# Kernel optimization log

Hardware: AMD Instinct MI355X
Metric: run time of the kernel (lower is better)

The kernel has to match this reference:

```python
import jax, jax.numpy as jnp
import numpy as np

NHEADS = 16


def setup_inputs() -> dict:
    key = jax.random.key(0)
    ks = jax.random.split(key, 5)
    B, S, D = 2, 2048, 1024
    x = jax.random.normal(ks[0], (B, S, D), dtype=jnp.float32)
    W_packed = jax.random.normal(ks[1], (3 * D, D), dtype=jnp.float32) * (1.0 / np.sqrt(D))
    b_packed = jax.random.normal(ks[2], (3 * D,), dtype=jnp.float32) * 0.02
    W_out = jax.random.normal(ks[3], (D, D), dtype=jnp.float32) * (1.0 / np.sqrt(D))
    b_out = jax.random.normal(ks[4], (D,), dtype=jnp.float32) * 0.02
    return {"x": x, "W_packed": W_packed, "b_packed": b_packed, "W_out": W_out, "b_out": b_out}


def reference(x, W_packed, b_packed, W_out, b_out):
    B, S, D = x.shape
    H = NHEADS
    hd = D // H
    # packed QKV projection (self-attention: q is k is v)
    qkv = x @ W_packed.T + b_packed                       # [B,S,3D]
    q, k, v = jnp.split(qkv, 3, axis=-1)

    def heads(t):
        return t.reshape(B, S, H, hd).transpose(0, 2, 1, 3)  # [B,H,S,hd]

    q, k, v = map(heads, (q, k, v))

    # ALiBi slopes per flex path: exp2(-(h+1)*8/H)
    slopes = jnp.exp2(-(jnp.arange(1, H + 1, dtype=x.dtype) * (8.0 / H)))  # [H]
    pos = jnp.arange(S)
    rel = (pos[None, :] - pos[:, None]).astype(x.dtype)    # kv_idx - q_idx, [S,S]
    bias = slopes[:, None, None] * rel                     # [H,S,S]
    causal = pos[None, :] <= pos[:, None]                  # allowed positions
    neg = jnp.finfo(x.dtype).min
    attn_mask = jnp.where(causal[None, :, :], bias, neg)   # [H,S,S]

    scale = 1.0 / np.sqrt(hd)
    scores = jnp.einsum("bhqd,bhkd->bhqk", q, k) * scale + attn_mask[None]
    attn = jax.nn.softmax(scores, axis=-1)
    out = jnp.einsum("bhqk,bhkd->bhqd", attn, v)           # [B,H,S,hd]
    out = out.transpose(0, 2, 1, 3).reshape(B, S, D)
    return out @ W_out.T + b_out
```

## Files before the change

kernel.cpp:

```cpp
#include <hip/hip_runtime.h>

typedef float f32x4 __attribute__((ext_vector_type(4)));
typedef __bf16 bf16x8 __attribute__((ext_vector_type(8)));
typedef unsigned short u16;

__device__ __forceinline__ f32x4 mfma16(bf16x8 a, bf16x8 b, f32x4 c) {
  return __builtin_amdgcn_mfma_f32_16x16x32_bf16(a, b, c, 0, 0, 0);
}

__device__ __forceinline__ void gll16(const void* g, void* l) {
  __builtin_amdgcn_global_load_lds(
      (const __attribute__((address_space(1))) void*)g,
      (__attribute__((address_space(3))) void*)l, 16, 0, 0);
}

__global__ void cvt_kernel(const float* __restrict__ in, __bf16* __restrict__ out, int n8) {
  int idx = blockIdx.x * blockDim.x + threadIdx.x;
  int stride = gridDim.x * blockDim.x;
  for (int i = idx; i < n8; i += stride) {
    const float* p = in + (size_t)i * 8;
    f32x4 a = *(const f32x4*)p;
    f32x4 b = *(const f32x4*)(p + 4);
    bf16x8 r;
#pragma unroll
    for (int j = 0; j < 4; ++j) {
      r[j] = (__bf16)a[j];
      r[4 + j] = (__bf16)b[j];
    }
    *(bf16x8*)(out + (size_t)i * 8) = r;
  }
}

template <int BM, int BN, int MODE>
__global__ __launch_bounds__(256, 4) void gemm_bt(
    const u16* __restrict__ A, const u16* __restrict__ B,
    const float* __restrict__ bias, float* __restrict__ Cout,
    __bf16* __restrict__ qb, __bf16* __restrict__ kp, __bf16* __restrict__ vp,
    int M, int N, int K, int mtiles) {
  constexpr int MREP = BM / 32;
  constexpr int NREP = BN / 32;
  constexpr int LA = BM / 64;
  constexpr int LB = BN / 64;
  __shared__ u16 lA[2 * BM * 32];
  __shared__ u16 lB[2 * BN * 32];
  const int tid = threadIdx.x;
  const int wid = tid >> 6;
  const int lane = tid & 63;
  const int lr = lane & 15;
  const int lg = lane >> 4;

  const int nwg = gridDim.x;
  const int lid = blockIdx.x;
  const int sw = (lid & 7) * (nwg >> 3) + (lid >> 3);
  const int bm = (sw % mtiles) * BM;
  const int bn = (sw / mtiles) * BN;

  const int wm = (wid >> 1) * (BM / 2);
  const int wn = (wid & 1) * (BN / 2);

  f32x4 acc[MREP][NREP] = {};

  auto stage = [&](int bf, int kt) {
    char* baseA = (char*)lA + bf * (BM * 64);
    char* baseB = (char*)lB + bf * (BN * 64);
#pragma unroll
    for (int j = 0; j < LA; ++j) {
      int off = (tid + j * 256) * 16;
      gll16(A + (size_t)(bm + (off >> 6)) * K + kt + ((off & 63) >> 1),
            baseA + off);
    }
#pragma unroll
    for (int j = 0; j < LB; ++j) {
      int off = (tid + j * 256) * 16;
      gll16(B + (size_t)(bn + (off >> 6)) * K + kt + ((off & 63) >> 1),
            baseB + off);
    }
  };

  int buf = 0;
  stage(0, 0);
  for (int kt = 0; kt < K; kt += 32) {
    __syncthreads();
    if (kt + 32 < K) stage(buf ^ 1, kt + 32);
    const u16* cA = lA + buf * BM * 32;
    const u16* cB = lB + buf * BN * 32;
    bf16x8 af[MREP], bfr[NREP];
#pragma unroll
    for (int mt = 0; mt < MREP; ++mt)
      af[mt] = *(const bf16x8*)&cA[(wm + mt * 16 + lr) * 32 + lg * 8];
#pragma unroll
    for (int nt = 0; nt < NREP; ++nt)
      bfr[nt] = *(const bf16x8*)&cB[(wn + nt * 16 + lr) * 32 + lg * 8];
#pragma unroll
    for (int mt = 0; mt < MREP; ++mt)
#pragma unroll
      for (int nt = 0; nt < NREP; ++nt)
        acc[mt][nt] = mfma16(af[mt], bfr[nt], acc[mt][nt]);
    buf ^= 1;
  }

#pragma unroll
  for (int nt = 0; nt < NREP; ++nt) {
    int col = bn + wn + nt * 16 + lr;
    float bv = bias[col];
#pragma unroll
    for (int mt = 0; mt < MREP; ++mt) {
#pragma unroll
      for (int r = 0; r < 4; ++r) {
        int row = bm + wm + mt * 16 + lg * 4 + r;
        float val = acc[mt][nt][r] + bv;
        if (MODE == 0) {
          Cout[(size_t)row * N + col] = val;
        } else {
          __bf16 bx = (__bf16)val;
          int b = row >> 11, s = row & 2047;
          int third = col >> 10, hd = col & 1023;
          int h = hd >> 6, d = hd & 63;
          if (third == 0) {
            qb[(size_t)row * 1024 + hd] = bx;
          } else {
            int bh = b * 16 + h, t = s >> 6, sr = s & 63;
            size_t tb = ((size_t)(bh * 32 + t)) * 4096;
            if (third == 1)
              kp[tb + (sr >> 4) * 1024 + (d >> 5) * 512 + ((d >> 3) & 3) * 128 +
                 (sr & 15) * 8 + (d & 7)] = bx;
            else
              vp[tb + (d >> 4) * 1024 + (sr >> 5) * 512 + ((sr >> 3) & 3) * 128 +
                 (d & 15) * 8 + (sr & 7)] = bx;
          }
        }
      }
    }
  }
}

__global__ __launch_bounds__(64, 4) void attn_kernel(
    const __bf16* __restrict__ qb, const __bf16* __restrict__ kp,
    const __bf16* __restrict__ vp, __bf16* __restrict__ aout) {
  __shared__ __bf16 p_lds[16][72];
  const int lane = threadIdx.x & 63;
  const int lr = lane & 15;
  const int lg = lane >> 4;

  const int lid = blockIdx.x;
  const int xcd = lid & 7;
  const int rest = lid >> 3;
  const int bh = xcd * 4 + (rest & 3);
  const int a16 = 127 - (rest >> 2);
  const int b = bh >> 4, h = bh & 15;
  const int qr0 = a16 * 16;
  const int ntl = (a16 >> 2) + 1;

  const float LOG2E = 1.4426950408889634f;
  const float c1 = 0.125f * LOG2E;
  const float c2 = exp2f(-(float)(h + 1) * 0.5f) * LOG2E;

  bf16x8 ones;
#pragma unroll
  for (int j = 0; j < 8; ++j) ones[j] = (__bf16)1.0f;

  const u16* ktiles = (const u16*)kp + (size_t)bh * 32 * 4096;
  const u16* vtiles = (const u16*)vp + (size_t)bh * 32 * 4096;

  const __bf16* qrow = qb + (size_t)(b * 2048 + qr0 + lr) * 1024 + h * 64;
  bf16x8 qf0 = *(const bf16x8*)(qrow + lg * 8);
  bf16x8 qf1 = *(const bf16x8*)(qrow + 32 + lg * 8);

  float m[4], l[4], cq[4];
  f32x4 o[4];
#pragma unroll
  for (int r = 0; r < 4; ++r) {
    m[r] = 0.f;
    l[r] = 0.f;
    cq[r] = c2 * (float)(qr0 + lg * 4 + r);
  }
#pragma unroll
  for (int dt = 0; dt < 4; ++dt) o[dt] = (f32x4){0.f, 0.f, 0.f, 0.f};

  for (int t = 0; t < ntl; ++t) {
    const u16* kb = ktiles + (size_t)t * 4096;
    const u16* vb = vtiles + (size_t)t * 4096;
    const int kv = t * 64;
    const bool last = (t == ntl - 1);

    bf16x8 ka[8], va[8];
#pragma unroll
    for (int j = 0; j < 8; ++j)
      ka[j] = *(const bf16x8*)(kb + j * 512 + lane * 8);
#pragma unroll
    for (int j = 0; j < 8; ++j)
      va[j] = *(const bf16x8*)(vb + j * 512 + lane * 8);

    f32x4 s[4];
#pragma unroll
    for (int nt = 0; nt < 4; ++nt) {
      f32x4 tt = (f32x4){0.f, 0.f, 0.f, 0.f};
      tt = mfma16(qf0, ka[nt * 2], tt);
      tt = mfma16(qf1, ka[nt * 2 + 1], tt);
      s[nt] = tt;
    }

#pragma unroll
    for (int nt = 0; nt < 4; ++nt) {
      float bnt = c2 * (float)(kv + nt * 16 + lr);
#pragma unroll
      for (int r = 0; r < 4; ++r)
        s[nt][r] = __builtin_fmaf(s[nt][r], c1, bnt - cq[r]);
    }
    if (last) {
#pragma unroll
      for (int nt = 0; nt < 4; ++nt) {
        float kf = (float)(kv + nt * 16 + lr);
#pragma unroll
        for (int r = 0; r < 4; ++r) {
          float qi = (float)(qr0 + lg * 4 + r);
          if (kf > qi) s[nt][r] = -1e30f;
        }
      }
    }

    float pm[4];
#pragma unroll
    for (int r = 0; r < 4; ++r)
      pm[r] = fmaxf(fmaxf(s[0][r], s[1][r]), fmaxf(s[2][r], s[3][r]));
    bool ok = (pm[0] <= m[0] + 8.f) && (pm[1] <= m[1] + 8.f) &&
              (pm[2] <= m[2] + 8.f) && (pm[3] <= m[3] + 8.f);
    if (!__all(ok)) {
#pragma unroll
      for (int r = 0; r < 4; ++r)
#pragma unroll
        for (int d = 1; d < 16; d <<= 1)
          pm[r] = fmaxf(pm[r], __shfl_xor(pm[r], d));
#pragma unroll
      for (int r = 0; r < 4; ++r) {
        float mn = fmaxf(m[r], pm[r]);
        float fac = __builtin_amdgcn_exp2f(m[r] - mn);
        m[r] = mn;
        l[r] *= fac;
#pragma unroll
        for (int dt = 0; dt < 4; ++dt) o[dt][r] *= fac;
      }
    }

#pragma unroll
    for (int nt = 0; nt < 4; ++nt)
#pragma unroll
      for (int r = 0; r < 4; ++r) {
        float e = __builtin_amdgcn_exp2f(s[nt][r] - m[r]);
        p_lds[lg * 4 + r][nt * 16 + lr] = (__bf16)e;
      }

    bf16x8 pa0 = *(const bf16x8*)&p_lds[lr][lg * 8];
    bf16x8 pa1 = *(const bf16x8*)&p_lds[lr][32 + lg * 8];

    {
      f32x4 tt = (f32x4){0.f, 0.f, 0.f, 0.f};
      tt = mfma16(pa0, ones, tt);
      tt = mfma16(pa1, ones, tt);
#pragma unroll
      for (int r = 0; r < 4; ++r) l[r] += tt[r];
    }

#pragma unroll
    for (int dt = 0; dt < 4; ++dt) {
      o[dt] = mfma16(pa0, va[dt * 2], o[dt]);
      o[dt] = mfma16(pa1, va[dt * 2 + 1], o[dt]);
    }
  }

#pragma unroll
  for (int dt = 0; dt < 4; ++dt)
#pragma unroll
    for (int r = 0; r < 4; ++r) {
      float val = o[dt][r] / l[r];
      aout[(size_t)(b * 2048 + qr0 + lg * 4 + r) * 1024 + h * 64 + dt * 16 + lr] =
          (__bf16)val;
    }
}

extern "C" void kernel_launch(void* const* d_in, const int* in_sizes, int n_in,
                              void* d_out, int out_size, void* d_ws, size_t ws_size,
                              hipStream_t stream) {
  (void)in_sizes; (void)n_in; (void)out_size; (void)ws_size;
  const float* x = (const float*)d_in[0];
  const float* Wp = (const float*)d_in[1];
  const float* bp = (const float*)d_in[2];
  const float* Wo = (const float*)d_in[3];
  const float* bo = (const float*)d_in[4];
  float* out = (float*)d_out;

  char* ws = (char*)d_ws;
  u16* xb  = (u16*)(ws);
  u16* wpb = (u16*)(ws + (size_t)(8u << 20));
  u16* wob = (u16*)(ws + (size_t)(14u << 20));
  u16* qbp = (u16*)(ws + (size_t)(16u << 20));
  u16* kpp = (u16*)(ws + (size_t)(24u << 20));
  u16* vpp = (u16*)(ws + (size_t)(32u << 20));
  u16* ab  = xb;

  cvt_kernel<<<2048, 256, 0, stream>>>(x, (__bf16*)xb, 4096 * 1024 / 8);
  cvt_kernel<<<1536, 256, 0, stream>>>(Wp, (__bf16*)wpb, 3072 * 1024 / 8);
  cvt_kernel<<<512, 256, 0, stream>>>(Wo, (__bf16*)wob, 1024 * 1024 / 8);
  gemm_bt<128, 64, 1><<<1536, 256, 0, stream>>>(
      xb, wpb, bp, nullptr, (__bf16*)qbp, (__bf16*)kpp, (__bf16*)vpp,
      4096, 3072, 1024, 32);
  attn_kernel<<<4096, 64, 0, stream>>>(
      (const __bf16*)qbp, (const __bf16*)kpp, (const __bf16*)vpp, (__bf16*)ab);
  gemm_bt<64, 64, 0><<<1024, 256, 0, stream>>>(
      ab, wob, bo, out, nullptr, nullptr, nullptr, 4096, 1024, 1024, 64);
}
```

Before: 125.3 us.

## Triple-buffer GEMM K-loop with explicit vmcnt waits and enlarge tiles to 128x128

```diff
diff --git a/kernel.cpp b/kernel.cpp
--- a/kernel.cpp
+++ b/kernel.cpp
@@ -32,7 +32,7 @@
 }
 
 template <int BM, int BN, int MODE>
-__global__ __launch_bounds__(256, 4) void gemm_bt(
+__global__ __launch_bounds__(256, 3) void gemm_bt(
     const u16* __restrict__ A, const u16* __restrict__ B,
     const float* __restrict__ bias, float* __restrict__ Cout,
     __bf16* __restrict__ qb, __bf16* __restrict__ kp, __bf16* __restrict__ vp,
@@ -41,8 +41,9 @@
   constexpr int NREP = BN / 32;
   constexpr int LA = BM / 64;
   constexpr int LB = BN / 64;
-  __shared__ u16 lA[2 * BM * 32];
-  __shared__ u16 lB[2 * BN * 32];
+  static_assert(LA + LB == 4, "vmcnt literals assume 4 loads/wave/step");
+  __shared__ u16 lA[3 * BM * 32];
+  __shared__ u16 lB[3 * BN * 32];
   const int tid = threadIdx.x;
   const int wid = tid >> 6;
   const int lane = tid & 63;
@@ -60,7 +61,8 @@
 
   f32x4 acc[MREP][NREP] = {};
 
-  auto stage = [&](int bf, int kt) {
+  auto stage = [&](int bf, int t) {
+    const int kt = t * 32;
     char* baseA = (char*)lA + bf * (BM * 64);
     char* baseB = (char*)lB + bf * (BN * 64);
 #pragma unroll
@@ -77,13 +79,23 @@
     }
   };
 
-  int buf = 0;
+  const int T = K / 32;
   stage(0, 0);
-  for (int kt = 0; kt < K; kt += 32) {
-    __syncthreads();
-    if (kt + 32 < K) stage(buf ^ 1, kt + 32);
-    const u16* cA = lA + buf * BM * 32;
-    const u16* cB = lB + buf * BN * 32;
+  stage(1, 1);
+  stage(2, 2);
+
+  for (int t = 0; t < T; ++t) {
+    const int rem = T - 1 - t;
+    if (rem >= 2)
+      asm volatile("s_waitcnt vmcnt(8)" ::: "memory");
+    else if (rem == 1)
+      asm volatile("s_waitcnt vmcnt(4)" ::: "memory");
+    else
+      asm volatile("s_waitcnt vmcnt(0)" ::: "memory");
+    __builtin_amdgcn_s_barrier();
+
+    const u16* cA = lA + (t % 3) * BM * 32;
+    const u16* cB = lB + (t % 3) * BN * 32;
     bf16x8 af[MREP], bfr[NREP];
 #pragma unroll
     for (int mt = 0; mt < MREP; ++mt)
@@ -96,7 +108,10 @@
 #pragma unroll
       for (int nt = 0; nt < NREP; ++nt)
         acc[mt][nt] = mfma16(af[mt], bfr[nt], acc[mt][nt]);
-    buf ^= 1;
+
+    __builtin_amdgcn_sched_barrier(0);
+    __builtin_amdgcn_s_barrier();
+    if (t + 3 < T) stage(t % 3, t + 3);
   }
 
 #pragma unroll
@@ -119,8 +134,8 @@
           if (third == 0) {
             qb[(size_t)row * 1024 + hd] = bx;
           } else {
-            int bh = b * 16 + h, t = s >> 6, sr = s & 63;
-            size_t tb = ((size_t)(bh * 32 + t)) * 4096;
+            int bh = b * 16 + h, t2 = s >> 6, sr = s & 63;
+            size_t tb = ((size_t)(bh * 32 + t2)) * 4096;
             if (third == 1)
               kp[tb + (sr >> 4) * 1024 + (d >> 5) * 512 + ((d >> 3) & 3) * 128 +
                  (sr & 15) * 8 + (d & 7)] = bx;
@@ -301,11 +316,11 @@
   cvt_kernel<<<2048, 256, 0, stream>>>(x, (__bf16*)xb, 4096 * 1024 / 8);
   cvt_kernel<<<1536, 256, 0, stream>>>(Wp, (__bf16*)wpb, 3072 * 1024 / 8);
   cvt_kernel<<<512, 256, 0, stream>>>(Wo, (__bf16*)wob, 1024 * 1024 / 8);
-  gemm_bt<128, 64, 1><<<1536, 256, 0, stream>>>(
+  gemm_bt<128, 128, 1><<<768, 256, 0, stream>>>(
       xb, wpb, bp, nullptr, (__bf16*)qbp, (__bf16*)kpp, (__bf16*)vpp,
       4096, 3072, 1024, 32);
   attn_kernel<<<4096, 64, 0, stream>>>(
       (const __bf16*)qbp, (const __bf16*)kpp, (const __bf16*)vpp, (__bf16*)ab);
-  gemm_bt<64, 64, 0><<<1024, 256, 0, stream>>>(
-      ab, wob, bo, out, nullptr, nullptr, nullptr, 4096, 1024, 1024, 64);
-}
+  gemm_bt<128, 128, 0><<<256, 256, 0, stream>>>(
+      ab, wob, bo, out, nullptr, nullptr, nullptr, 4096, 1024, 1024, 32);
+}
```

New measurement: 120.5 us. 1.04x faster.
